# Optimization experiments

Measured on AMD Instinct MI355X. Metric: run time of the kernel, lower is better.

The kernel has to match this reference:

```python
import jax, jax.numpy as jnp
import numpy as np

DIM = 256
NUM_HEADS = 8
HEAD_DIM = DIM // NUM_HEADS
KERNEL_SIZES = (5, 7, 9)
DILATIONS = (1, 2, 3)
HEADS_PER_RANGE = (4, 3, 1)  # replicates torch allocation: weights~1/k^2, floor + greedy remainder
SCALE = HEAD_DIM ** -0.5


def _unfold(x, ks, dil):
    # x: (B, h, d, H, W) -> (B, h, d, L, H, W), L = ks*ks, same-padded dilated neighborhood gather
    B, h, d, H, W = x.shape
    pad = (ks // 2) * dil
    xp = jnp.pad(x, ((0, 0), (0, 0), (0, 0), (pad, pad), (pad, pad)))
    patches = [xp[..., i * dil:i * dil + H, j * dil:j * dil + W]
               for i in range(ks) for j in range(ks)]
    return jnp.stack(patches, axis=3)


def _attend_range(q, k, v, ks, dil, rpb):
    # q,k,v: (B, h_i, d, H, W); rpb: (h_i, L)
    k_nb = _unfold(k, ks, dil)  # (B,h,d,L,H,W)
    v_nb = _unfold(v, ks, dil)
    logits = jnp.einsum('bhdxy,bhdlxy->bhlxy', q * SCALE, k_nb)
    logits = logits + rpb[None, :, :, None, None]
    attn = jax.nn.softmax(logits, axis=2)
    return jnp.einsum('bhlxy,bhdlxy->bhdxy', attn, v_nb)


def setup_inputs() -> dict:
    key = jax.random.key(0)
    ks = jax.random.split(key, 6)
    B, C, H, W = 4, DIM, 64, 64
    s = 0.02
    inp = {
        'x': jax.random.normal(ks[0], (B, C, H, W), dtype=jnp.float32),
        'qkv_w': jax.random.normal(ks[1], (3 * DIM, DIM), dtype=jnp.float32) * s,
        'qkv_b': jnp.zeros((3 * DIM,), dtype=jnp.float32),
        'proj_w': jax.random.normal(ks[2], (DIM, DIM), dtype=jnp.float32) * s,
        'proj_b': jnp.zeros((DIM,), dtype=jnp.float32),
    }
    for i, kk in enumerate(KERNEL_SIZES):
        inp[f'rpb{i}'] = jax.random.normal(ks[3 + i], (HEADS_PER_RANGE[i], kk * kk), dtype=jnp.float32) * s
    return inp


def reference(x, qkv_w, qkv_b, proj_w, proj_b, rpb0, rpb1, rpb2):
    B, C, H, W = x.shape
    qkv = jnp.einsum('oc,bcxy->boxy', qkv_w, x) + qkv_b[None, :, None, None]
    q, k, v = jnp.split(qkv, 3, axis=1)
    q = q.reshape(B, NUM_HEADS, HEAD_DIM, H, W)
    k = k.reshape(B, NUM_HEADS, HEAD_DIM, H, W)
    v = v.reshape(B, NUM_HEADS, HEAD_DIM, H, W)
    rpbs = (rpb0, rpb1, rpb2)
    outs = []
    hs = 0
    for i in range(len(KERNEL_SIZES)):
        he = hs + HEADS_PER_RANGE[i]
        outs.append(_attend_range(q[:, hs:he], k[:, hs:he], v[:, hs:he],
                                  KERNEL_SIZES[i], DILATIONS[i], rpbs[i]))
        hs = he
    out = jnp.concatenate(outs, axis=1).reshape(B, C, H, W)
    out = jnp.einsum('oc,bcxy->boxy', proj_w, out) + proj_b[None, :, None, None]
    return out
```

## Files before the change

kernel.cpp:

```cpp
#include <hip/hip_runtime.h>
#include <math.h>

#define H_IMG 64
#define W_IMG 64
#define PIX   (H_IMG * W_IMG)
#define NB    4
#define NHEADS 8
#define HD    32
#define CDIM  256
#define QKV_C 768
#define ATT_SCALE 0.17677669529663687f

typedef _Float16 half8_t __attribute__((ext_vector_type(8)));
typedef _Float16 half2_t __attribute__((ext_vector_type(2)));
typedef float f32x4 __attribute__((ext_vector_type(4)));

__global__ void cvt_w16(const float* __restrict__ a, int na,
                        const float* __restrict__ b, int nb,
                        _Float16* __restrict__ da, _Float16* __restrict__ db) {
    int i = blockIdx.x * 256 + threadIdx.x;
    if (i < na) da[i] = (_Float16)a[i];
    else if (i - na < nb) db[i - na] = (_Float16)b[i - na];
}

__launch_bounds__(256)
__global__ void transpose_to_f16(const float* __restrict__ src,
                                 _Float16* __restrict__ dst, int C) {
    __shared__ _Float16 tl[64][66];
    const int b  = blockIdx.z;
    const int p0 = blockIdx.x * 64;
    const int c0 = blockIdx.y * 64;
    const int tx = threadIdx.x;
    const int ty = threadIdx.y;
    const float* s = src + (size_t)b * C * PIX;
    _Float16* d = dst + (size_t)b * PIX * C;
#pragma unroll
    for (int cc = ty; cc < 64; cc += 4)
        tl[cc][tx] = (_Float16)s[(size_t)(c0 + cc) * PIX + p0 + tx];
    __syncthreads();
#pragma unroll
    for (int pp = ty; pp < 64; pp += 4)
        d[(size_t)(p0 + pp) * C + c0 + tx] = tl[tx][pp];
}

template <typename OutT, bool PAIR>
__launch_bounds__(256)
__global__ void gemm16(const _Float16* __restrict__ A,
                       const _Float16* __restrict__ BT,
                       const float* __restrict__ bias,
                       OutT* __restrict__ Y,
                       int M, int K, int N) {
    __shared__ _Float16 Asl[128][40];
    __shared__ _Float16 Bsl[128][40];
    const int b = blockIdx.z;
    const _Float16* Bb = BT + (size_t)b * N * K;
    OutT* Yb = Y + (size_t)b * M * N;
    const int m0 = blockIdx.y * 128;
    const int n0 = blockIdx.x * 128;
    const int t    = threadIdx.x;
    const int lane = t & 63;
    const int w    = t >> 6;
    const int wm = w >> 1, wn = w & 1;
    const int l15 = lane & 15;
    const int kq  = (lane >> 4) * 8;

    f32x4 acc[4][4];
#pragma unroll
    for (int mt = 0; mt < 4; mt++)
#pragma unroll
        for (int nt = 0; nt < 4; nt++)
            acc[mt][nt] = (f32x4){0.f, 0.f, 0.f, 0.f};

    for (int k0 = 0; k0 < K; k0 += 32) {
        __syncthreads();
#pragma unroll
        for (int i = 0; i < 2; i++) {
            int idx = t + i * 256;
            int row = idx >> 2;
            int seg = (idx & 3) * 8;
            *(half8_t*)&Asl[row][seg] = *(const half8_t*)(A  + (size_t)(m0 + row) * K + k0 + seg);
            *(half8_t*)&Bsl[row][seg] = *(const half8_t*)(Bb + (size_t)(n0 + row) * K + k0 + seg);
        }
        __syncthreads();
        half8_t af[4], bf[4];
#pragma unroll
        for (int mt = 0; mt < 4; mt++)
            af[mt] = *(const half8_t*)&Asl[wm * 64 + mt * 16 + l15][kq];
#pragma unroll
        for (int nt = 0; nt < 4; nt++)
            bf[nt] = *(const half8_t*)&Bsl[wn * 64 + nt * 16 + l15][kq];
#pragma unroll
        for (int mt = 0; mt < 4; mt++)
#pragma unroll
            for (int nt = 0; nt < 4; nt++)
                acc[mt][nt] = __builtin_amdgcn_mfma_f32_16x16x32_f16(
                    af[mt], bf[nt], acc[mt][nt], 0, 0, 0);
    }

    const int rq = lane >> 4;
    if constexpr (PAIR) {
        unsigned* Yp = (unsigned*)Yb;
#pragma unroll
        for (int mt = 0; mt < 4; mt++) {
#pragma unroll
            for (int s = 0; s < 2; s++) {
                int mp = m0 + wm * 64 + mt * 16 + rq * 4 + 2 * s;
                float b0 = bias[mp], b1 = bias[mp + 1];
#pragma unroll
                for (int nt = 0; nt < 4; nt++) {
                    int col = n0 + wn * 64 + nt * 16 + l15;
                    half2_t hv;
                    hv.x = (_Float16)(acc[mt][nt][2 * s]     + b0);
                    hv.y = (_Float16)(acc[mt][nt][2 * s + 1] + b1);
                    Yp[(size_t)(mp >> 1) * N + col] = __builtin_bit_cast(unsigned, hv);
                }
            }
        }
    } else {
#pragma unroll
        for (int mt = 0; mt < 4; mt++) {
#pragma unroll
            for (int r = 0; r < 4; r++) {
                int m = m0 + wm * 64 + mt * 16 + rq * 4 + r;
                float bs = bias[m];
                OutT* yp = Yb + (size_t)m * N + n0 + wn * 64;
#pragma unroll
                for (int nt = 0; nt < 4; nt++)
                    yp[nt * 16 + l15] = (OutT)(acc[mt][nt][r] + bs);
            }
        }
    }
}

template <int KS, int DIL>
__device__ __forceinline__ void attn_wave(const unsigned* __restrict__ base,
                                          const float* __restrict__ rp,
                                          _Float16* __restrict__ outp,
                                          int h, int y) {
    const int x = threadIdx.x;

    const unsigned* qb = base + (size_t)(h * 16) * PIX + y * W_IMG + x;
    const unsigned* kb = base + (size_t)(128 + h * 16) * PIX + x;
    const unsigned* vb = base + (size_t)(256 + h * 16) * PIX + x;

    half2_t qh[16];
#pragma unroll
    for (int d2 = 0; d2 < 16; d2++)
        qh[d2] = __builtin_bit_cast(half2_t, qb[(size_t)d2 * PIX]);

    float acc[HD];
#pragma unroll
    for (int d = 0; d < HD; d++) acc[d] = 0.f;
    float denom = 0.f;

#pragma unroll 1
    for (int i = 0; i < KS; i++) {
        const int yy = y + (i - KS / 2) * DIL;
        const float* rrow = rp + i * KS;
        if ((unsigned)yy < (unsigned)H_IMG) {
            int kr[16], vr[16];
            const unsigned* ko = kb + yy * W_IMG;
            const unsigned* vo = vb + yy * W_IMG;
#pragma unroll
            for (int d2 = 0; d2 < 16; d2++) {
                kr[d2] = (int)ko[(size_t)d2 * PIX];
                vr[d2] = (int)vo[(size_t)d2 * PIX];
            }
#pragma unroll
            for (int j = 0; j < KS; j++) {
                const int xx = x + (j - KS / 2) * DIL;
                const int src = xx & 63;
                const bool vx = (unsigned)xx < (unsigned)W_IMG;
                float s0 = 0.f, s1 = 0.f, s2 = 0.f, s3 = 0.f;
#pragma unroll
                for (int d2 = 0; d2 < 16; d2 += 4) {
                    half2_t k0 = __builtin_bit_cast(half2_t, __shfl(kr[d2 + 0], src));
                    half2_t k1 = __builtin_bit_cast(half2_t, __shfl(kr[d2 + 1], src));
                    half2_t k2 = __builtin_bit_cast(half2_t, __shfl(kr[d2 + 2], src));
                    half2_t k3 = __builtin_bit_cast(half2_t, __shfl(kr[d2 + 3], src));
#if __has_builtin(__builtin_amdgcn_fdot2)
                    s0 = __builtin_amdgcn_fdot2(qh[d2 + 0], k0, s0, false);
                    s1 = __builtin_amdgcn_fdot2(qh[d2 + 1], k1, s1, false);
                    s2 = __builtin_amdgcn_fdot2(qh[d2 + 2], k2, s2, false);
                    s3 = __builtin_amdgcn_fdot2(qh[d2 + 3], k3, s3, false);
#else
                    s0 += (float)qh[d2+0].x * (float)k0.x + (float)qh[d2+0].y * (float)k0.y;
                    s1 += (float)qh[d2+1].x * (float)k1.x + (float)qh[d2+1].y * (float)k1.y;
                    s2 += (float)qh[d2+2].x * (float)k2.x + (float)qh[d2+2].y * (float)k2.y;
                    s3 += (float)qh[d2+3].x * (float)k3.x + (float)qh[d2+3].y * (float)k3.y;
#endif
                }
                const float rb = rrow[j];
                float logit = fmaf((s0 + s1) + (s2 + s3), ATT_SCALE, rb);
                logit = vx ? logit : rb;
                const float wgt = __expf(logit);
                denom += wgt;
                const float wv = vx ? wgt : 0.f;
#pragma unroll
                for (int d2 = 0; d2 < 16; d2++) {
                    half2_t vv = __builtin_bit_cast(half2_t, __shfl(vr[d2], src));
                    acc[2 * d2]     += wv * (float)vv.x;
                    acc[2 * d2 + 1] += wv * (float)vv.y;
                }
            }
        } else {
#pragma unroll
            for (int j = 0; j < KS; j++) denom += __expf(rrow[j]);
        }
    }

    const float inv = 1.f / denom;
#pragma unroll
    for (int g = 0; g < 4; g++) {
        half8_t hv;
#pragma unroll
        for (int e = 0; e < 8; e++) hv[e] = (_Float16)(acc[g * 8 + e] * inv);
        *(half8_t*)(outp + g * 8) = hv;
    }
}

__launch_bounds__(256)
__global__ void attn_v4(const unsigned* __restrict__ qkv,
                        const float* __restrict__ rpb0,
                        const float* __restrict__ rpb1,
                        const float* __restrict__ rpb2,
                        _Float16* __restrict__ outT) {
    const int b = blockIdx.x >> 3;
    const int h = blockIdx.x & 7;
    const int y = blockIdx.y * 4 + threadIdx.y;

    const unsigned* base = qkv + (size_t)b * (QKV_C / 2) * PIX;
    const int p = y * W_IMG + threadIdx.x;
    _Float16* outp = outT + ((size_t)b * PIX + p) * CDIM + h * HD;

    if (h < 4) {
        attn_wave<5, 1>(base, rpb0 + h * 25, outp, h, y);
    } else if (h < 7) {
        attn_wave<7, 2>(base, rpb1 + (h - 4) * 49, outp, h, y);
    } else {
        attn_wave<9, 3>(base, rpb2, outp, h, y);
    }
}

extern "C" void kernel_launch(void* const* d_in, const int* in_sizes, int n_in,
                              void* d_out, int out_size, void* d_ws, size_t ws_size,
                              hipStream_t stream) {
    const float* x      = (const float*)d_in[0];
    const float* qkv_w  = (const float*)d_in[1];
    const float* qkv_b  = (const float*)d_in[2];
    const float* proj_w = (const float*)d_in[3];
    const float* proj_b = (const float*)d_in[4];
    const float* rpb0   = (const float*)d_in[5];
    const float* rpb1   = (const float*)d_in[6];
    const float* rpb2   = (const float*)d_in[7];
    float* out = (float*)d_out;

    char* ws = (char*)d_ws;
    _Float16* qkv16 = (_Float16*)ws;
    _Float16* T16   = (_Float16*)(ws + (size_t)NB * QKV_C * PIX * 2);
    _Float16* W16   = T16 + (size_t)NB * PIX * CDIM;
    _Float16* P16   = W16 + (size_t)QKV_C * CDIM;

    const int nw = QKV_C * CDIM, np = CDIM * CDIM;
    cvt_w16<<<dim3((nw + np + 255) / 256), dim3(256), 0, stream>>>(qkv_w, nw, proj_w, np, W16, P16);

    transpose_to_f16<<<dim3(PIX / 64, CDIM / 64, NB), dim3(64, 4), 0, stream>>>(x, T16, CDIM);

    gemm16<_Float16, true><<<dim3(PIX / 128, QKV_C / 128, NB), dim3(256), 0, stream>>>(
        W16, T16, qkv_b, qkv16, QKV_C, CDIM, PIX);

    attn_v4<<<dim3(NB * NHEADS, H_IMG / 4), dim3(64, 4), 0, stream>>>(
        (const unsigned*)qkv16, rpb0, rpb1, rpb2, T16);

    gemm16<float, false><<<dim3(PIX / 128, CDIM / 128, NB), dim3(256), 0, stream>>>(
        P16, T16, proj_b, out, CDIM, CDIM, PIX);
}
```

Baseline: 176.8 us.

## Split large-kernel attention heads across waves and merge partials in LDS

The attention kernel now launches one block per (batch, image row) with 13 waves. The 5x5 heads keep one wave each, while each 7x7 head is split over 2 waves and the 9x9 head over 3 waves by ranges of kernel rows. Partial accumulators and softmax denominators go to shared memory and are summed after a barrier. The aim is to even out per-wave work and remove the tail from the long 9x9 head, at the cost of a large LDS buffer (about 76 KB), a 832-thread block that limits occupancy, and an extra reduction step.

```diff
diff --git a/kernel.cpp b/kernel.cpp
--- a/kernel.cpp
+++ b/kernel.cpp
@@ -133,10 +133,11 @@
 }
 
 template <int KS, int DIL>
-__device__ __forceinline__ void attn_wave(const unsigned* __restrict__ base,
+__device__ __forceinline__ void attn_part(const unsigned* __restrict__ base,
                                           const float* __restrict__ rp,
-                                          _Float16* __restrict__ outp,
-                                          int h, int y) {
+                                          int h, int y, int i0, int i1,
+                                          float* __restrict__ acc,
+                                          float& denom) {
     const int x = threadIdx.x;
 
     const unsigned* qb = base + (size_t)(h * 16) * PIX + y * W_IMG + x;
@@ -148,13 +149,8 @@
     for (int d2 = 0; d2 < 16; d2++)
         qh[d2] = __builtin_bit_cast(half2_t, qb[(size_t)d2 * PIX]);
 
-    float acc[HD];
-#pragma unroll
-    for (int d = 0; d < HD; d++) acc[d] = 0.f;
-    float denom = 0.f;
-
 #pragma unroll 1
-    for (int i = 0; i < KS; i++) {
+    for (int i = i0; i < i1; i++) {
         const int yy = y + (i - KS / 2) * DIL;
         const float* rrow = rp + i * KS;
         if ((unsigned)yy < (unsigned)H_IMG) {
@@ -208,37 +204,81 @@
             for (int j = 0; j < KS; j++) denom += __expf(rrow[j]);
         }
     }
-
+}
+
+__device__ __forceinline__ void store_attn(_Float16* __restrict__ op,
+                                           const float* __restrict__ acc,
+                                           float denom) {
     const float inv = 1.f / denom;
 #pragma unroll
     for (int g = 0; g < 4; g++) {
         half8_t hv;
 #pragma unroll
         for (int e = 0; e < 8; e++) hv[e] = (_Float16)(acc[g * 8 + e] * inv);
-        *(half8_t*)(outp + g * 8) = hv;
-    }
-}
-
-__launch_bounds__(256)
-__global__ void attn_v4(const unsigned* __restrict__ qkv,
+        *(half8_t*)(op + g * 8) = hv;
+    }
+}
+
+__launch_bounds__(832)
+__global__ void attn_v5(const unsigned* __restrict__ qkv,
                         const float* __restrict__ rpb0,
                         const float* __restrict__ rpb1,
                         const float* __restrict__ rpb2,
                         _Float16* __restrict__ outT) {
-    const int b = blockIdx.x >> 3;
-    const int h = blockIdx.x & 7;
-    const int y = blockIdx.y * 4 + threadIdx.y;
+    __shared__ float P[9][33][64];
+    const int b  = blockIdx.x;
+    const int y  = blockIdx.y;
+    const int x  = threadIdx.x;
+    const int ty = threadIdx.y;
 
     const unsigned* base = qkv + (size_t)b * (QKV_C / 2) * PIX;
-    const int p = y * W_IMG + threadIdx.x;
-    _Float16* outp = outT + ((size_t)b * PIX + p) * CDIM + h * HD;
-
-    if (h < 4) {
-        attn_wave<5, 1>(base, rpb0 + h * 25, outp, h, y);
-    } else if (h < 7) {
-        attn_wave<7, 2>(base, rpb1 + (h - 4) * 49, outp, h, y);
+    const int p = y * W_IMG + x;
+
+    float acc[HD];
+#pragma unroll
+    for (int d = 0; d < HD; d++) acc[d] = 0.f;
+    float denom = 0.f;
+
+    int h;
+    int slot = -1;
+    if (ty < 4) {
+        h = ty;
+        attn_part<5, 1>(base, rpb0 + h * 25, h, y, 0, 5, acc, denom);
+    } else if (ty < 10) {
+        const int idx = ty - 4;
+        h = 4 + (idx >> 1);
+        const int half = idx & 1;
+        attn_part<7, 2>(base, rpb1 + (h - 4) * 49, h, y, half ? 4 : 0, half ? 7 : 4, acc, denom);
+        slot = idx;
     } else {
-        attn_wave<9, 3>(base, rpb2, outp, h, y);
+        h = 7;
+        const int t3 = ty - 10;
+        attn_part<9, 3>(base, rpb2, h, y, 3 * t3, 3 * t3 + 3, acc, denom);
+        slot = 6 + t3;
+    }
+
+    _Float16* op = outT + ((size_t)b * PIX + p) * CDIM + h * HD;
+
+    if (slot < 0) {
+        store_attn(op, acc, denom);
+    } else {
+#pragma unroll
+        for (int d = 0; d < HD; d++) P[slot][d][x] = acc[d];
+        P[slot][HD][x] = denom;
+    }
+    __syncthreads();
+
+    if (ty == 4 || ty == 6 || ty == 8) {
+        const int s0 = ty - 4;
+        float m[HD];
+#pragma unroll
+        for (int d = 0; d < HD; d++) m[d] = P[s0][d][x] + P[s0 + 1][d][x];
+        store_attn(op, m, P[s0][HD][x] + P[s0 + 1][HD][x]);
+    } else if (ty == 10) {
+        float m[HD];
+#pragma unroll
+        for (int d = 0; d < HD; d++) m[d] = P[6][d][x] + P[7][d][x] + P[8][d][x];
+        store_attn(op, m, P[6][HD][x] + P[7][HD][x] + P[8][HD][x]);
     }
 }
 
@@ -269,7 +309,7 @@
     gemm16<_Float16, true><<<dim3(PIX / 128, QKV_C / 128, NB), dim3(256), 0, stream>>>(
         W16, T16, qkv_b, qkv16, QKV_C, CDIM, PIX);
 
-    attn_v4<<<dim3(NB * NHEADS, H_IMG / 4), dim3(64, 4), 0, stream>>>(
+    attn_v5<<<dim3(NB, H_IMG), dim3(64, 13), 0, stream>>>(
         (const unsigned*)qkv16, rpb0, rpb1, rpb2, T16);
 
     gemm16<float, false><<<dim3(PIX / 128, CDIM / 128, NB), dim3(256), 0, stream>>>(
```

After: 152.6 us. 1.16x faster.
